# Kernel tuning notes

Measured on AMD Instinct MI355X. Metric: run time of the kernel, lower is better.

Reference implementation:

```python
import jax, jax.numpy as jnp
import numpy as np

B, T, D, H, HD = 2, 2048, 1024, 16, 64
NEG_INF = jnp.float32(-1e30)


def setup_inputs() -> dict:
    key = jax.random.key(0)
    ks = jax.random.split(key, 6)
    scale = 0.02
    return {
        "x": jax.random.normal(ks[0], (B, T, D), dtype=jnp.float32),
        "Wq": jax.random.normal(ks[1], (H, D, HD), dtype=jnp.float32) * scale,
        "Wk": jax.random.normal(ks[2], (H, D, HD), dtype=jnp.float32) * scale,
        "Wv": jax.random.normal(ks[3], (H, D, HD), dtype=jnp.float32) * scale,
        "Wp": jax.random.normal(ks[4], (D, H * HD), dtype=jnp.float32) * scale,
        "bp": jnp.zeros((D,), dtype=jnp.float32),
    }


def reference(x, Wq, Wk, Wv, Wp, bp):
    # Per-head QKV projections (stacked over heads): [B,H,T,HD]
    q = jnp.einsum("btd,hde->bhte", x, Wq)
    k = jnp.einsum("btd,hde->bhte", x, Wk)
    v = jnp.einsum("btd,hde->bhte", x, Wv)
    # Scaled scores [B,H,T,T] with causal mask, stable softmax
    scores = jnp.einsum("bhte,bhse->bhts", q, k) * (HD ** -0.5)
    causal = jnp.tril(jnp.ones((T, T), dtype=bool))
    scores = jnp.where(causal, scores, NEG_INF)
    attn = jax.nn.softmax(scores, axis=-1)
    out = jnp.einsum("bhts,bhse->bhte", attn, v)
    # Concat heads: [B,T,H*HD], then output projection (torch Linear: y = x @ W.T + b)
    concat = out.transpose(0, 2, 1, 3).reshape(B, T, H * HD)
    return concat @ Wp.T + bp
```

## Files before the change

### kernel.cpp

```cpp
#include <hip/hip_runtime.h>
#include <hip/hip_bf16.h>

#define TSEQ 2048
#define DM   1024
#define NH   16
#define HDIM 64
#define NB   2
#define BT   (NB*TSEQ)
#define QSCALE 0.1803368801111204f

typedef __attribute__((ext_vector_type(8))) short bf16x8;
typedef __attribute__((ext_vector_type(4))) float f32x4;

union BF8 { bf16x8 v; ushort u[8]; };

static __device__ __forceinline__ ushort f2b(float x) {
    unsigned u = __float_as_uint(x);
    return (ushort)((u + 0x7fff + ((u >> 16) & 1)) >> 16);
}

static __device__ __forceinline__ unsigned cvtpk(float lo, float hi) {
    unsigned r;
    asm("v_cvt_pk_bf16_f32 %0, %1, %2" : "=v"(r) : "v"(lo), "v"(hi));
    return r;
}

static __device__ __forceinline__ float fmax3(float a, float b, float c) {
    return fmaxf(fmaxf(a, b), c);
}

static __device__ __forceinline__ void gload16(const void* g, void* l) {
    __builtin_amdgcn_global_load_lds((const __attribute__((address_space(1))) void*)g,
                                     (__attribute__((address_space(3))) void*)l, 16, 0, 0);
}

__global__ __launch_bounds__(256) void prep_kernel(const float* __restrict__ x,
                                                   const float* __restrict__ Wq,
                                                   const float* __restrict__ Wk,
                                                   const float* __restrict__ Wv,
                                                   const float* __restrict__ Wp,
                                                   ushort* __restrict__ xb,
                                                   ushort* __restrict__ wpb,
                                                   ushort* __restrict__ wtb) {
    __shared__ float tile[64][65];
    const int g = blockIdx.x, t = threadIdx.x;
    if (g < 2560) {
        const float* src = (g < 2048) ? x : Wp;
        ushort* dst = (g < 2048) ? xb : wpb;
        int i = ((g < 2048) ? g : (g - 2048)) * 256 + t;
        const float4* s = reinterpret_cast<const float4*>(src);
        float4 a = s[2*i], b = s[2*i+1];
        union { ushort u[8]; int4 v; } r;
        r.u[0]=f2b(a.x); r.u[1]=f2b(a.y); r.u[2]=f2b(a.z); r.u[3]=f2b(a.w);
        r.u[4]=f2b(b.x); r.u[5]=f2b(b.y); r.u[6]=f2b(b.z); r.u[7]=f2b(b.w);
        reinterpret_cast<int4*>(dst)[i] = r.v;
        return;
    }
    const int gb = g - 2560;
    const int k0 = (gb & 15) * 64;
    const int math = gb >> 4;
    const int mat = math >> 4, h = math & 15;
    const float* W = (mat == 0 ? Wq : (mat == 1 ? Wk : Wv)) + (size_t)h * DM * HDIM;
#pragma unroll
    for (int it = 0; it < 4; ++it) {
        int row = it*16 + (t>>4), c4 = (t&15)*4;
        float4 v = *reinterpret_cast<const float4*>(&W[(size_t)(k0+row)*HDIM + c4]);
        tile[row][c4+0]=v.x; tile[row][c4+1]=v.y; tile[row][c4+2]=v.z; tile[row][c4+3]=v.w;
    }
    __syncthreads();
    ushort* out = wtb + (size_t)(mat*NH + h) * (HDIM*DM);
#pragma unroll
    for (int it = 0; it < 4; ++it) {
        int n = it*16 + (t>>4), kc = (t&15)*4;
        union { ushort u[4]; uint2 v; } r;
#pragma unroll
        for (int j = 0; j < 4; ++j) r.u[j] = f2b(tile[kc+j][n]);
        *reinterpret_cast<uint2*>(&out[(size_t)n*DM + k0 + kc]) = r.v;
    }
}

template<int EPI>
__global__ __launch_bounds__(256) void gemm_bt(const ushort* __restrict__ A,
                                               const ushort* __restrict__ B,
                                               const float* __restrict__ bias,
                                               void* __restrict__ C) {
    __shared__ ushort As[128*64];
    __shared__ ushort Bs[128*64];
    const int tid = threadIdx.x;
    const int w = tid >> 6, l = tid & 63;
    const int lr = l & 15, lg = l >> 4;
    const int wr = (w >> 1) * 64, wc = (w & 1) * 64;
    const int cpx = (int)gridDim.x >> 3;
    const int wg = ((int)blockIdx.x & 7) * cpx + ((int)blockIdx.x >> 3);
    const int m0 = (wg & 31) * 128;
    const int n0 = (wg >> 5) * 128;
    const int srow = l >> 3;
    const int scol = (l & 7) * 8;

    f32x4 acc[4][4];
#pragma unroll
    for (int a = 0; a < 4; ++a)
#pragma unroll
        for (int b = 0; b < 4; ++b) acc[a][b] = {0.f, 0.f, 0.f, 0.f};

    for (int kc = 0; kc < DM/64; ++kc) {
        __syncthreads();
#pragma unroll
        for (int c = 0; c < 4; ++c) {
            int chunk = w*4 + c;
            int r = chunk*8 + srow;
            gload16(&A[(size_t)(m0+r)*DM + kc*64 + scol], &As[chunk*512]);
            gload16(&B[(size_t)(n0+r)*DM + kc*64 + scol], &Bs[chunk*512]);
        }
        __syncthreads();
#pragma unroll
        for (int kk = 0; kk < 2; ++kk) {
            bf16x8 af[4], bf[4];
#pragma unroll
            for (int mf = 0; mf < 4; ++mf)
                af[mf] = *reinterpret_cast<const bf16x8*>(&As[(wr + mf*16 + lr)*64 + kk*32 + lg*8]);
#pragma unroll
            for (int nf = 0; nf < 4; ++nf)
                bf[nf] = *reinterpret_cast<const bf16x8*>(&Bs[(wc + nf*16 + lr)*64 + kk*32 + lg*8]);
            __builtin_amdgcn_s_setprio(1);
#pragma unroll
            for (int mf = 0; mf < 4; ++mf)
#pragma unroll
                for (int nf = 0; nf < 4; ++nf)
                    acc[mf][nf] = __builtin_amdgcn_mfma_f32_16x16x32_bf16(
                        af[mf], bf[nf], acc[mf][nf], 0, 0, 0);
            __builtin_amdgcn_s_setprio(0);
        }
    }

    if (EPI == 0) {
        ushort* O = (ushort*)C;
#pragma unroll
        for (int mf = 0; mf < 4; ++mf) {
#pragma unroll
            for (int i = 0; i < 4; ++i) {
                int m = m0 + wr + mf*16 + lg*4 + i;
                int bq = m >> 11, t = m & (TSEQ - 1);
#pragma unroll
                for (int nf = 0; nf < 4; ++nf) {
                    int col = n0 + wc + nf*16 + lr;
                    int mat = col >> 10, hh = (col >> 6) & 15, e = col & 63;
                    float sc = (mat == 0) ? QSCALE : 1.0f;
                    O[((size_t)(mat*2*NH + bq*NH + hh))*(TSEQ*HDIM) + (size_t)t*HDIM + e] =
                        f2b(acc[mf][nf][i] * sc);
                }
            }
        }
    } else {
        float* O = (float*)C;
#pragma unroll
        for (int mf = 0; mf < 4; ++mf) {
#pragma unroll
            for (int i = 0; i < 4; ++i) {
                int m = m0 + wr + mf*16 + lg*4 + i;
#pragma unroll
                for (int nf = 0; nf < 4; ++nf) {
                    int col = n0 + wc + nf*16 + lr;
                    O[(size_t)m*DM + col] = acc[mf][nf][i] + bias[col];
                }
            }
        }
    }
}

__global__ __launch_bounds__(512) void attn_mfma(const ushort* __restrict__ qkvb,
                                                 ushort* __restrict__ concatb) {
    __shared__ ushort Ks[2][64*64];
    __shared__ ushort Vt[2][64*64];
    __shared__ ushort Ps[8][16*64];
    const int tid = threadIdx.x;
    const int w = tid >> 6, l = tid & 63;
    const int lr = l & 15, lg = l >> 4;
    const int g = blockIdx.x;
    const int bh = (g & 7) * 4 + ((g >> 3) & 3);
    const int p  = g >> 5;
    const int qtHI = 16 + p, qtLO = 15 - p;
    const int sub = w >> 2;
    const int ws  = w & 3;
    const int myqt = sub ? qtLO : qtHI;
    const int q0 = myqt * 64 + ws * 16;

    const ushort* Q = qkvb + (size_t)bh * (TSEQ*HDIM);
    const ushort* K = Q + (size_t)2*NH*TSEQ*HDIM;
    const ushort* V = K + (size_t)2*NH*TSEQ*HDIM;

    bf16x8 qf[2];
#pragma unroll
    for (int kk = 0; kk < 2; ++kk)
        qf[kk] = *reinterpret_cast<const bf16x8*>(&Q[(size_t)(q0 + lr)*HDIM + kk*32 + lg*8]);

    f32x4 acc[4];
    float mrow = -3e38f, lrow = 0.f;
#pragma unroll
    for (int nf = 0; nf < 4; ++nf) acc[nf] = {0.f, 0.f, 0.f, 0.f};

    ushort* PsW = &Ps[w][0];
    const int krow = tid >> 3;
    const int kchunk = (tid & 7) ^ ((tid >> 3) & 7);

    {
        gload16(&K[(size_t)krow*HDIM + kchunk*8], &Ks[0][tid*8]);
        BF8 a;
        a.v = *reinterpret_cast<const bf16x8*>(&V[(size_t)l*HDIM + w*8]);
#pragma unroll
        for (int j = 0; j < 8; ++j)
            Vt[0][(w*8 + j)*64 + ((l>>3) ^ j)*8 + (l&7)] = a.u[j];
        __syncthreads();
    }

    int cur = 0;
    for (int jt = 0; jt <= qtHI; ++jt) {
        const int nxt = cur ^ 1;
        const int s0 = jt * 64;
        const bool pref = (jt < qtHI);
        const bool active = (sub == 0) || (jt <= qtLO);
        BF8 ga;
        if (pref) {
            const int s0n = s0 + 64;
            gload16(&K[(size_t)(s0n + krow)*HDIM + kchunk*8], &Ks[nxt][tid*8]);
            ga.v = *reinterpret_cast<const bf16x8*>(&V[(size_t)(s0n + l)*HDIM + w*8]);
        }

        if (active) {
            f32x4 sT[4];
#pragma unroll
            for (int nf = 0; nf < 4; ++nf) sT[nf] = {0.f, 0.f, 0.f, 0.f};
#pragma unroll
            for (int kk = 0; kk < 2; ++kk) {
                bf16x8 kf[4];
#pragma unroll
                for (int nf = 0; nf < 4; ++nf)
                    kf[nf] = *reinterpret_cast<const bf16x8*>(
                        &Ks[cur][(nf*16 + lr)*64 + ((kk*4 + lg) ^ (lr&7))*8]);
                __builtin_amdgcn_s_setprio(1);
#pragma unroll
                for (int nf = 0; nf < 4; ++nf)
                    sT[nf] = __builtin_amdgcn_mfma_f32_16x16x32_bf16(kf[nf], qf[kk], sT[nf], 0, 0, 0);
                __builtin_amdgcn_s_setprio(0);
            }
            if (jt == myqt) {
                int qrow = q0 + lr;
#pragma unroll
                for (int nf = 0; nf < 4; ++nf) {
                    int kbase = s0 + nf*16 + lg*4;
#pragma unroll
                    for (int i = 0; i < 4; ++i)
                        if (kbase + i > qrow) sT[nf][i] = -1e30f;
                }
            }
            float g0 = fmax3(sT[0][0], sT[0][1], sT[0][2]);
            float g1 = fmax3(sT[0][3], sT[1][0], sT[1][1]);
            float g2 = fmax3(sT[1][2], sT[1][3], sT[2][0]);
            float g3 = fmax3(sT[2][1], sT[2][2], sT[2][3]);
            float g4 = fmax3(sT[3][0], sT[3][1], sT[3][2]);
            float tm = fmaxf(fmax3(fmax3(g0, g1, g2), g3, g4), sT[3][3]);
            if (__any(tm > mrow + 8.0f)) {
                tm = fmaxf(tm, __shfl_xor(tm, 16, 64));
                tm = fmaxf(tm, __shfl_xor(tm, 32, 64));
                float mnew = fmaxf(mrow, tm);
                float corr = exp2f(mrow - mnew);
                lrow *= corr;
#pragma unroll
                for (int nf = 0; nf < 4; ++nf)
#pragma unroll
                    for (int i = 0; i < 4; ++i) acc[nf][i] *= corr;
                mrow = mnew;
            }
            float ps = 0.f;
#pragma unroll
            for (int nf = 0; nf < 4; ++nf)
#pragma unroll
                for (int i = 0; i < 4; ++i) { sT[nf][i] = exp2f(sT[nf][i] - mrow); ps += sT[nf][i]; }
            lrow += ps;
#pragma unroll
            for (int nf = 0; nf < 4; ++nf) {
                uint2 pk;
                pk.x = cvtpk(sT[nf][0], sT[nf][1]);
                pk.y = cvtpk(sT[nf][2], sT[nf][3]);
                *reinterpret_cast<uint2*>(
                    &PsW[lr*64 + ((2*nf + (lg>>1)) ^ (lr&7))*8 + (lg&1)*4]) = pk;
            }
#pragma unroll
            for (int kk = 0; kk < 2; ++kk) {
                bf16x8 vf[4];
#pragma unroll
                for (int nf = 0; nf < 4; ++nf)
                    vf[nf] = *reinterpret_cast<const bf16x8*>(
                        &Vt[cur][(nf*16 + lr)*64 + ((kk*4 + lg) ^ (lr&7))*8]);
                bf16x8 pf = *reinterpret_cast<const bf16x8*>(
                    &PsW[lr*64 + ((kk*4 + lg) ^ (lr&7))*8]);
                __builtin_amdgcn_s_setprio(1);
#pragma unroll
                for (int nf = 0; nf < 4; ++nf)
                    acc[nf] = __builtin_amdgcn_mfma_f32_16x16x32_bf16(vf[nf], pf, acc[nf], 0, 0, 0);
                __builtin_amdgcn_s_setprio(0);
            }
        }

        if (pref) {
#pragma unroll
            for (int j = 0; j < 8; ++j)
                Vt[nxt][(w*8 + j)*64 + ((l>>3) ^ j)*8 + (l&7)] = ga.u[j];
        }
        __syncthreads();
        cur = nxt;
    }

    lrow += __shfl_xor(lrow, 16, 64);
    lrow += __shfl_xor(lrow, 32, 64);
    const int b = bh >> 4, h = bh & 15;
    {
        float inv = 1.0f / lrow;
        int t = q0 + lr;
        ushort* o = concatb + ((size_t)(b*TSEQ + t))*DM + h*HDIM;
#pragma unroll
        for (int nf = 0; nf < 4; ++nf) {
            uint2 pk;
            pk.x = cvtpk(acc[nf][0]*inv, acc[nf][1]*inv);
            pk.y = cvtpk(acc[nf][2]*inv, acc[nf][3]*inv);
            *reinterpret_cast<uint2*>(&o[nf*16 + lg*4]) = pk;
        }
    }
}

extern "C" void kernel_launch(void* const* d_in, const int* in_sizes, int n_in,
                              void* d_out, int out_size, void* d_ws, size_t ws_size,
                              hipStream_t stream) {
    const float* x  = (const float*)d_in[0];
    const float* Wq = (const float*)d_in[1];
    const float* Wk = (const float*)d_in[2];
    const float* Wv = (const float*)d_in[3];
    const float* Wp = (const float*)d_in[4];
    const float* bp = (const float*)d_in[5];
    float* out = (float*)d_out;

    ushort* ws   = (ushort*)d_ws;
    ushort* xb   = ws;
    ushort* wtb  = xb  + (size_t)BT*DM;
    ushort* wpb  = wtb + (size_t)3*NH*HDIM*DM;
    ushort* qkvb = wpb + (size_t)DM*DM;
    ushort* cb   = qkvb + (size_t)3*2*NH*TSEQ*HDIM;

    prep_kernel<<<dim3(3328), 256, 0, stream>>>(x, Wq, Wk, Wv, Wp, xb, wpb, wtb);
    gemm_bt<0><<<dim3(32*24), 256, 0, stream>>>(xb, wtb, nullptr, qkvb);
    attn_mfma<<<dim3(512), 512, 0, stream>>>(qkvb, cb);
    gemm_bt<1><<<dim3(32*8), 256, 0, stream>>>(cb, wpb, bp, out);
}
```

Baseline: 122.1 us.

## Write V transposed from projection GEMM and load it directly into LDS

The QKV projection is split in two. A new EPI==2 GEMM variant computes the V part with swapped MFMA operands and stores V in [e][t] transposed layout. The attention kernel can then fetch V tiles with direct global-to-LDS loads, replacing the register load followed by a scalar transpose scatter into shared memory. The cost is an extra kernel launch and strided 2-byte scattered stores in the V epilogue, and it relies on the swizzle pattern staying consistent with the Vt reads.

```diff
diff --git a/kernel.cpp b/kernel.cpp
--- a/kernel.cpp
+++ b/kernel.cpp
@@ -11,8 +11,6 @@
 
 typedef __attribute__((ext_vector_type(8))) short bf16x8;
 typedef __attribute__((ext_vector_type(4))) float f32x4;
-
-union BF8 { bf16x8 v; ushort u[8]; };
 
 static __device__ __forceinline__ ushort f2b(float x) {
     unsigned u = __float_as_uint(x);
@@ -126,9 +124,14 @@
 #pragma unroll
             for (int mf = 0; mf < 4; ++mf)
 #pragma unroll
-                for (int nf = 0; nf < 4; ++nf)
-                    acc[mf][nf] = __builtin_amdgcn_mfma_f32_16x16x32_bf16(
-                        af[mf], bf[nf], acc[mf][nf], 0, 0, 0);
+                for (int nf = 0; nf < 4; ++nf) {
+                    if (EPI == 2)
+                        acc[mf][nf] = __builtin_amdgcn_mfma_f32_16x16x32_bf16(
+                            bf[nf], af[mf], acc[mf][nf], 0, 0, 0);
+                    else
+                        acc[mf][nf] = __builtin_amdgcn_mfma_f32_16x16x32_bf16(
+                            af[mf], bf[nf], acc[mf][nf], 0, 0, 0);
+                }
             __builtin_amdgcn_s_setprio(0);
         }
     }
@@ -148,6 +151,23 @@
                     float sc = (mat == 0) ? QSCALE : 1.0f;
                     O[((size_t)(mat*2*NH + bq*NH + hh))*(TSEQ*HDIM) + (size_t)t*HDIM + e] =
                         f2b(acc[mf][nf][i] * sc);
+                }
+            }
+        }
+    } else if (EPI == 2) {
+        ushort* O = (ushort*)C;
+#pragma unroll
+        for (int mf = 0; mf < 4; ++mf) {
+            int tglob = m0 + wr + mf*16 + lr;
+            int bq = tglob >> 11, tt = tglob & (TSEQ - 1);
+#pragma unroll
+            for (int nf = 0; nf < 4; ++nf) {
+#pragma unroll
+                for (int i = 0; i < 4; ++i) {
+                    int n = n0 + wc + nf*16 + lg*4 + i;
+                    int hh = n >> 6, e = n & 63;
+                    O[((size_t)(4*NH + bq*NH + hh))*(TSEQ*HDIM) + (size_t)e*TSEQ + tt] =
+                        f2b(acc[mf][nf][i]);
                 }
             }
         }
@@ -185,9 +205,9 @@
     const int myqt = sub ? qtLO : qtHI;
     const int q0 = myqt * 64 + ws * 16;
 
-    const ushort* Q = qkvb + (size_t)bh * (TSEQ*HDIM);
-    const ushort* K = Q + (size_t)2*NH*TSEQ*HDIM;
-    const ushort* V = K + (size_t)2*NH*TSEQ*HDIM;
+    const ushort* Q  = qkvb + (size_t)bh * (TSEQ*HDIM);
+    const ushort* K  = Q + (size_t)2*NH*TSEQ*HDIM;
+    const ushort* VT = K + (size_t)2*NH*TSEQ*HDIM;
 
     bf16x8 qf[2];
 #pragma unroll
@@ -204,12 +224,8 @@
     const int kchunk = (tid & 7) ^ ((tid >> 3) & 7);
 
     {
-        gload16(&K[(size_t)krow*HDIM + kchunk*8], &Ks[0][tid*8]);
-        BF8 a;
-        a.v = *reinterpret_cast<const bf16x8*>(&V[(size_t)l*HDIM + w*8]);
-#pragma unroll
-        for (int j = 0; j < 8; ++j)
-            Vt[0][(w*8 + j)*64 + ((l>>3) ^ j)*8 + (l&7)] = a.u[j];
+        gload16(&K [(size_t)krow*HDIM + kchunk*8], &Ks[0][tid*8]);
+        gload16(&VT[(size_t)krow*TSEQ + kchunk*8], &Vt[0][tid*8]);
         __syncthreads();
     }
 
@@ -219,11 +235,10 @@
         const int s0 = jt * 64;
         const bool pref = (jt < qtHI);
         const bool active = (sub == 0) || (jt <= qtLO);
-        BF8 ga;
         if (pref) {
             const int s0n = s0 + 64;
-            gload16(&K[(size_t)(s0n + krow)*HDIM + kchunk*8], &Ks[nxt][tid*8]);
-            ga.v = *reinterpret_cast<const bf16x8*>(&V[(size_t)(s0n + l)*HDIM + w*8]);
+            gload16(&K [(size_t)(s0n + krow)*HDIM + kchunk*8], &Ks[nxt][tid*8]);
+            gload16(&VT[(size_t)krow*TSEQ + s0n + kchunk*8], &Vt[nxt][tid*8]);
         }
 
         if (active) {
@@ -302,11 +317,6 @@
             }
         }
 
-        if (pref) {
-#pragma unroll
-            for (int j = 0; j < 8; ++j)
-                Vt[nxt][(w*8 + j)*64 + ((l>>3) ^ j)*8 + (l&7)] = ga.u[j];
-        }
         __syncthreads();
         cur = nxt;
     }
@@ -345,9 +355,11 @@
     ushort* wpb  = wtb + (size_t)3*NH*HDIM*DM;
     ushort* qkvb = wpb + (size_t)DM*DM;
     ushort* cb   = qkvb + (size_t)3*2*NH*TSEQ*HDIM;
+    const ushort* wtbv = wtb + (size_t)2*NH*HDIM*DM;
 
     prep_kernel<<<dim3(3328), 256, 0, stream>>>(x, Wq, Wk, Wv, Wp, xb, wpb, wtb);
-    gemm_bt<0><<<dim3(32*24), 256, 0, stream>>>(xb, wtb, nullptr, qkvb);
+    gemm_bt<0><<<dim3(32*16), 256, 0, stream>>>(xb, wtb, nullptr, qkvb);
+    gemm_bt<2><<<dim3(32*8), 256, 0, stream>>>(xb, wtbv, nullptr, qkvb);
     attn_mfma<<<dim3(512), 512, 0, stream>>>(qkvb, cb);
     gemm_bt<1><<<dim3(32*8), 256, 0, stream>>>(cb, wpb, bp, out);
 }
```

Result: slower. 137.9 us (+13.0%).
